# Performance work log

Measured on AMD Instinct MI355X. Metric: run time of the kernel, lower is better.

Reference implementation:

```python
import jax, jax.numpy as jnp
import numpy as np

N, D, H, C = 50000, 256, 4, 16  # nodes, in_dim, heads, out_channels (hidden_dim)
E = 1600000
NEG_SLOPE = 0.2


def _gatv2_layer(x, src, dst, Wl, bl, Wr, br, att, bias, n_nodes):
    """PyG GATv2Conv (share_weights=False, concat=True, eval mode).
    x: [N, Fin]; Wl/Wr: [Fin, H*C]; att: [H, C]; bias: [H*C].
    """
    xl = (x @ Wl + bl).reshape(n_nodes, H, C)  # source-side transform
    xr = (x @ Wr + br).reshape(n_nodes, H, C)  # target-side transform
    # per-edge attention logits: a^T LeakyReLU(xl_j + xr_i)
    e = jax.nn.leaky_relu(xl[src] + xr[dst], negative_slope=NEG_SLOPE)  # [E,H,C]
    logits = jnp.einsum('ehc,hc->eh', e, att)  # [E,H]
    # scatter-softmax over incoming edges of each target node
    m = jax.ops.segment_max(logits, dst, num_segments=n_nodes)  # [N,H]
    ex = jnp.exp(logits - m[dst])
    denom = jax.ops.segment_sum(ex, dst, num_segments=n_nodes)  # [N,H]
    alpha = ex / denom[dst]  # [E,H]
    out = jax.ops.segment_sum(alpha[:, :, None] * xl[src], dst, num_segments=n_nodes)
    return out.reshape(n_nodes, H * C) + bias


def setup_inputs() -> dict:
    key = jax.random.key(0)
    ks = jax.random.split(key, 16)
    g = lambda k, shp, fan: jax.random.normal(k, shp, jnp.float32) * (1.0 / np.sqrt(fan))
    inp = {
        'x': jax.random.normal(ks[0], (N, D), jnp.float32),
        'edge_index': jax.random.randint(ks[1], (2, E), 0, N, dtype=jnp.int64),
        # conv1: in D -> H*C
        'Wl1': g(ks[2], (D, H * C), D), 'bl1': jnp.zeros((H * C,), jnp.float32),
        'Wr1': g(ks[3], (D, H * C), D), 'br1': jnp.zeros((H * C,), jnp.float32),
        'att1': g(ks[4], (H, C), C), 'bias1': jnp.zeros((H * C,), jnp.float32),
        # conv2: in H*C -> H*C
        'Wl2': g(ks[5], (H * C, H * C), H * C), 'bl2': jnp.zeros((H * C,), jnp.float32),
        'Wr2': g(ks[6], (H * C, H * C), H * C), 'br2': jnp.zeros((H * C,), jnp.float32),
        'att2': g(ks[7], (H, C), C), 'bias2': jnp.zeros((H * C,), jnp.float32),
        # output head: H*C -> D
        'Wo': g(ks[8], (H * C, D), H * C), 'bo': jnp.zeros((D,), jnp.float32),
    }
    return inp


def reference(x, edge_index, Wl1, bl1, Wr1, br1, att1, bias1,
              Wl2, bl2, Wr2, br2, att2, bias2, Wo, bo):
    src, dst = edge_index[0], edge_index[1]
    h = jax.nn.relu(_gatv2_layer(x, src, dst, Wl1, bl1, Wr1, br1, att1, bias1, N))
    h = jax.nn.relu(_gatv2_layer(h, src, dst, Wl2, bl2, Wr2, br2, att2, bias2, N))
    return jax.nn.sigmoid(h @ Wo + bo)  # min_max is None -> no affine rescale
```

## Files before the change

### kernel.cpp

```cpp
#include <hip/hip_runtime.h>
#include <math.h>

#define NN 50000
#define DIN 256
#define HC 64
#define NEG 0.2f
#define TM 64
#define NB 196
#define EPB 4096
#define CAP 36864

typedef short bf16x8 __attribute__((ext_vector_type(8)));
typedef unsigned short ush8 __attribute__((ext_vector_type(8)));
typedef float f32x4 __attribute__((ext_vector_type(4)));

__device__ __forceinline__ unsigned short f2bf(float x) {
    unsigned u = __float_as_uint(x);
    u += 0x7FFFu + ((u >> 16) & 1u);
    return (unsigned short)(u >> 16);
}
__device__ __forceinline__ float bf2f(unsigned short h) {
    return __uint_as_float((unsigned)h << 16);
}

template <int CTRL>
__device__ __forceinline__ float dpp_mov(float x) {
    int r = __builtin_amdgcn_update_dpp(0, __float_as_int(x), CTRL, 0xF, 0xF, true);
    return __int_as_float(r);
}


__global__ __launch_bounds__(256) void bhist_k(const int* __restrict__ dst,
                                               int* __restrict__ bcnt, int E) {
    __shared__ int h[NB];
    int t = threadIdx.x;
    for (int i = t; i < NB; i += 256) h[i] = 0;
    __syncthreads();
    int base = blockIdx.x * 2048 + t;
#pragma unroll
    for (int k = 0; k < 8; ++k) {
        int e = base + k * 256;
        if (e < E) atomicAdd(&h[dst[e] >> 8], 1);
    }
    __syncthreads();
    for (int i = t; i < NB; i += 256)
        if (h[i]) atomicAdd(&bcnt[i], h[i]);
}

__global__ __launch_bounds__(256) void bscan_k(const int* __restrict__ bcnt,
                                               int* __restrict__ boffs,
                                               int* __restrict__ bcursor,
                                               int* __restrict__ offs, int E) {
    __shared__ int s[256];
    int t = threadIdx.x;
    s[t] = (t < NB) ? bcnt[t] : 0;
    __syncthreads();
    for (int off = 1; off < 256; off <<= 1) {
        int v = s[t];
        int u = (t >= off) ? s[t - off] : 0;
        __syncthreads();
        s[t] = v + u;
        __syncthreads();
    }
    if (t < NB) {
        int ex = (t == 0) ? 0 : s[t - 1];
        boffs[t] = ex;
        bcursor[t] = ex;
    }
    if (t == NB) boffs[NB] = s[NB - 1];
    if (t == 0) offs[NN] = E;
}

__global__ __launch_bounds__(1024) void bin_k(const int* __restrict__ src,
                                              const int* __restrict__ dst,
                                              int* __restrict__ bcursor,
                                              unsigned* __restrict__ epair, int E) {
    __shared__ int hist[NB];
    __shared__ int lofs[NB];
    __shared__ int gshift[NB];
    __shared__ int scanb[256];
    __shared__ unsigned pbuf[EPB];
    __shared__ unsigned char abkt[EPB];
    int t = threadIdx.x;
    for (int i = t; i < NB; i += 1024) hist[i] = 0;
    __syncthreads();
    int e0 = blockIdx.x * EPB;
    unsigned p[4]; int bk[4], rk[4]; bool val[4];
#pragma unroll
    for (int k = 0; k < 4; ++k) {
        int e = e0 + k * 1024 + t;
        val[k] = e < E;
        if (val[k]) {
            int s = src[e], d = dst[e];
            p[k] = ((unsigned)s << 8) | (unsigned)(d & 255);
            bk[k] = d >> 8;
            rk[k] = atomicAdd(&hist[bk[k]], 1);
        }
    }
    __syncthreads();
    if (t < 256) scanb[t] = (t < NB) ? hist[t] : 0;
    __syncthreads();
    for (int off = 1; off < 256; off <<= 1) {
        int v = 0, u = 0;
        if (t < 256) { v = scanb[t]; if (t >= off) u = scanb[t - off]; }
        __syncthreads();
        if (t < 256) scanb[t] = v + u;
        __syncthreads();
    }
    if (t < NB) {
        int ex = (t == 0) ? 0 : scanb[t - 1];
        lofs[t] = ex;
        int gb = atomicAdd(&bcursor[t], hist[t]);
        gshift[t] = gb - ex;
    }
    __syncthreads();
    int total = scanb[NB - 1];
#pragma unroll
    for (int k = 0; k < 4; ++k) {
        if (val[k]) {
            int pos = lofs[bk[k]] + rk[k];
            pbuf[pos] = p[k];
            abkt[pos] = (unsigned char)bk[k];
        }
    }
    __syncthreads();
    for (int i = t; i < total; i += 1024) {
        int b = abkt[i];
        epair[gshift[b] + i] = pbuf[i];
    }
}

__global__ __launch_bounds__(1024) void bsort_k(const unsigned* __restrict__ epair,
                                                const int* __restrict__ boffs,
                                                int* __restrict__ offs,
                                                unsigned* __restrict__ ssrc, int n) {
    __shared__ int lhist[256];
    __shared__ int lcur[256];
    __shared__ int scanb[256];
    __shared__ unsigned sbuf[CAP];
    int b = blockIdx.x, t = threadIdx.x;
    int start = boffs[b], end = boffs[b + 1];
    int cnt = end - start;
    if (t < 256) lhist[t] = 0;
    __syncthreads();
    for (int i = t; i < cnt; i += 1024) {
        unsigned p = epair[start + i];
        atomicAdd(&lhist[p & 255], 1);
    }
    __syncthreads();
    if (t < 256) scanb[t] = lhist[t];
    __syncthreads();
    for (int off = 1; off < 256; off <<= 1) {
        int v = 0, u = 0;
        if (t < 256) { v = scanb[t]; if (t >= off) u = scanb[t - off]; }
        __syncthreads();
        if (t < 256) scanb[t] = v + u;
        __syncthreads();
    }
    if (t < 256) {
        int ex = (t == 0) ? 0 : scanb[t - 1];
        lcur[t] = ex;
        int node = b * 256 + t;
        if (node < n) offs[node] = start + ex;
    }
    __syncthreads();
    if (cnt <= CAP) {
        for (int i = t; i < cnt; i += 1024) {
            unsigned p = epair[start + i];
            int r = atomicAdd(&lcur[p & 255], 1);
            sbuf[r] = p & ~255u;
        }
        __syncthreads();
        for (int i = t; i < cnt; i += 1024) ssrc[start + i] = sbuf[i];
    } else {
        for (int i = t; i < cnt; i += 1024) {
            unsigned p = epair[start + i];
            int r = atomicAdd(&lcur[p & 255], 1);
            ssrc[start + r] = p & ~255u;
        }
    }
}

__global__ __launch_bounds__(256) void wprep_dual_k(const float* __restrict__ Wl,
                                                    const float* __restrict__ Wr,
                                                    unsigned short* __restrict__ img,
                                                    int K) {
    int i = blockIdx.x * 256 + threadIdx.x;
    int total = (K >> 5) * 10240;
    if (i >= total) return;
    int kk = i % 40;
    int c  = (i / 40) & 127;
    int p  = (i / 5120) & 1;
    int s  = i / 10240;
    unsigned short v = 0;
    if (kk < 32) {
        int k = s * 32 + kk;
        float w = (c < 64) ? Wl[k * HC + c] : Wr[k * HC + (c - 64)];
        unsigned short hi = f2bf(w);
        v = p ? f2bf(w - bf2f(hi)) : hi;
    }
    img[i] = v;
}

__global__ __launch_bounds__(256) void wprep_head_k(const float* __restrict__ Wo,
                                                    unsigned short* __restrict__ img) {
    int i = blockIdx.x * 256 + threadIdx.x;
    if (i >= 40960) return;
    int kk = i % 40;
    int c  = (i / 40) & 127;
    int p  = (i / 5120) & 1;
    int s  = (i / 10240) & 1;
    int h  = i / 20480;
    unsigned short v = 0;
    if (kk < 32) {
        int k = s * 32 + kk;
        float w = Wo[k * DIN + h * 128 + c];
        unsigned short hi = f2bf(w);
        v = p ? f2bf(w - bf2f(hi)) : hi;
    }
    img[i] = v;
}

__global__ __launch_bounds__(256) void gemm_dual_mfma_k(
        const float* __restrict__ A,
        const unsigned short* __restrict__ img,
        const float* __restrict__ bl, const float* __restrict__ br,
        float* __restrict__ xl, float* __restrict__ xr,
        int n, int K) {
    __shared__ __attribute__((aligned(16))) unsigned short As[2][64][40];
    __shared__ __attribute__((aligned(16))) unsigned short Bs[2][128][40];
    int t = threadIdx.x;
    int l = t & 63, w = t >> 6;
    int wr = w >> 1, wc = w & 1;
    int lan = l & 15;
    int kb  = (l >> 4) * 8;
    int row0 = blockIdx.x * 64;
    int srow = t >> 2;
    int skq  = (t & 3) * 8;
    bool rok = (row0 + srow) < n;
    const float* aptr = A + (size_t)(row0 + srow) * K + skq;

    f32x4 acc0[4] = {}, acc1[4] = {};

    int nks = K >> 5;
    for (int ks = 0; ks < nks; ++ks) {
        __syncthreads();
        {
            const ush8* src = (const ush8*)(img + (size_t)ks * 10240);
            ush8* dst = (ush8*)&Bs[0][0][0];
            int base = w * 5 * 64 + l;
#pragma unroll
            for (int c2 = 0; c2 < 5; ++c2) {
                int u = base + c2 * 64;
                dst[u] = src[u];
            }
        }
        {
            float4 f0 = make_float4(0.f, 0.f, 0.f, 0.f), f1 = f0;
            if (rok) {
                f0 = *(const float4*)(aptr + ks * 32);
                f1 = *(const float4*)(aptr + ks * 32 + 4);
            }
            float xs[8] = {f0.x, f0.y, f0.z, f0.w, f1.x, f1.y, f1.z, f1.w};
            ush8 hi8, lo8;
#pragma unroll
            for (int j = 0; j < 8; ++j) {
                unsigned short h = f2bf(xs[j]);
                hi8[j] = h;
                lo8[j] = f2bf(xs[j] - bf2f(h));
            }
            *(ush8*)&As[0][srow][skq] = hi8;
            *(ush8*)&As[1][srow][skq] = lo8;
        }
        __syncthreads();
        bf16x8 ah0 = *(const bf16x8*)&As[0][wr * 32 + lan][kb];
        bf16x8 ah1 = *(const bf16x8*)&As[0][wr * 32 + 16 + lan][kb];
        bf16x8 al0 = *(const bf16x8*)&As[1][wr * 32 + lan][kb];
        bf16x8 al1 = *(const bf16x8*)&As[1][wr * 32 + 16 + lan][kb];
#pragma unroll
        for (int cf = 0; cf < 4; ++cf) {
            int bc = wc * 64 + cf * 16 + lan;
            bf16x8 bhv = *(const bf16x8*)&Bs[0][bc][kb];
            bf16x8 blv = *(const bf16x8*)&Bs[1][bc][kb];
            acc0[cf] = __builtin_amdgcn_mfma_f32_16x16x32_bf16(ah0, bhv, acc0[cf], 0, 0, 0);
            acc1[cf] = __builtin_amdgcn_mfma_f32_16x16x32_bf16(ah1, bhv, acc1[cf], 0, 0, 0);
            acc0[cf] = __builtin_amdgcn_mfma_f32_16x16x32_bf16(al0, bhv, acc0[cf], 0, 0, 0);
            acc1[cf] = __builtin_amdgcn_mfma_f32_16x16x32_bf16(al1, bhv, acc1[cf], 0, 0, 0);
            acc0[cf] = __builtin_amdgcn_mfma_f32_16x16x32_bf16(ah0, blv, acc0[cf], 0, 0, 0);
            acc1[cf] = __builtin_amdgcn_mfma_f32_16x16x32_bf16(ah1, blv, acc1[cf], 0, 0, 0);
        }
    }
#pragma unroll
    for (int cf = 0; cf < 4; ++cf) {
        int col = wc * 64 + cf * 16 + lan;
        float bv; float* dst; int c2;
        if (col < 64) { bv = bl[col]; dst = xl; c2 = col; }
        else          { bv = br[col - 64]; dst = xr; c2 = col - 64; }
#pragma unroll
        for (int rf = 0; rf < 2; ++rf) {
            f32x4 a = rf ? acc1[cf] : acc0[cf];
            int rbase = row0 + wr * 32 + rf * 16 + (l >> 4) * 4;
#pragma unroll
            for (int r = 0; r < 4; ++r) {
                int grow = rbase + r;
                if (grow < n) dst[(size_t)grow * HC + c2] = a[r] + bv;
            }
        }
    }
}

__global__ __launch_bounds__(256) void head_gemm_mfma_k(
        const float* __restrict__ A,
        const unsigned short* __restrict__ img,
        const float* __restrict__ bo,
        float* __restrict__ out, int n) {
    __shared__ __attribute__((aligned(16))) unsigned short As[2][64][40];
    __shared__ __attribute__((aligned(16))) unsigned short Bs[2][128][40];
    int t = threadIdx.x;
    int l = t & 63, w = t >> 6;
    int wr = w >> 1, wc = w & 1;
    int lan = l & 15;
    int kb  = (l >> 4) * 8;
    int row0 = blockIdx.x * 64;
    int coloff = blockIdx.y * 128;
    const unsigned short* himg = img + (size_t)blockIdx.y * 2 * 10240;
    int srow = t >> 2;
    int skq  = (t & 3) * 8;
    bool rok = (row0 + srow) < n;
    const float* aptr = A + (size_t)(row0 + srow) * HC + skq;

    f32x4 acc0[4] = {}, acc1[4] = {};

    for (int ks = 0; ks < 2; ++ks) {
        __syncthreads();
        {
            const ush8* src = (const ush8*)(himg + (size_t)ks * 10240);
            ush8* dst = (ush8*)&Bs[0][0][0];
            int base = w * 5 * 64 + l;
#pragma unroll
            for (int c2 = 0; c2 < 5; ++c2) {
                int u = base + c2 * 64;
                dst[u] = src[u];
            }
        }
        {
            float4 f0 = make_float4(0.f, 0.f, 0.f, 0.f), f1 = f0;
            if (rok) {
                f0 = *(const float4*)(aptr + ks * 32);
                f1 = *(const float4*)(aptr + ks * 32 + 4);
            }
            float xs[8] = {f0.x, f0.y, f0.z, f0.w, f1.x, f1.y, f1.z, f1.w};
            ush8 hi8, lo8;
#pragma unroll
            for (int j = 0; j < 8; ++j) {
                unsigned short h = f2bf(xs[j]);
                hi8[j] = h;
                lo8[j] = f2bf(xs[j] - bf2f(h));
            }
            *(ush8*)&As[0][srow][skq] = hi8;
            *(ush8*)&As[1][srow][skq] = lo8;
        }
        __syncthreads();
        bf16x8 ah0 = *(const bf16x8*)&As[0][wr * 32 + lan][kb];
        bf16x8 ah1 = *(const bf16x8*)&As[0][wr * 32 + 16 + lan][kb];
        bf16x8 al0 = *(const bf16x8*)&As[1][wr * 32 + lan][kb];
        bf16x8 al1 = *(const bf16x8*)&As[1][wr * 32 + 16 + lan][kb];
#pragma unroll
        for (int cf = 0; cf < 4; ++cf) {
            int bc = wc * 64 + cf * 16 + lan;
            bf16x8 bhv = *(const bf16x8*)&Bs[0][bc][kb];
            bf16x8 blv = *(const bf16x8*)&Bs[1][bc][kb];
            acc0[cf] = __builtin_amdgcn_mfma_f32_16x16x32_bf16(ah0, bhv, acc0[cf], 0, 0, 0);
            acc1[cf] = __builtin_amdgcn_mfma_f32_16x16x32_bf16(ah1, bhv, acc1[cf], 0, 0, 0);
            acc0[cf] = __builtin_amdgcn_mfma_f32_16x16x32_bf16(al0, bhv, acc0[cf], 0, 0, 0);
            acc1[cf] = __builtin_amdgcn_mfma_f32_16x16x32_bf16(al1, bhv, acc1[cf], 0, 0, 0);
            acc0[cf] = __builtin_amdgcn_mfma_f32_16x16x32_bf16(ah0, blv, acc0[cf], 0, 0, 0);
            acc1[cf] = __builtin_amdgcn_mfma_f32_16x16x32_bf16(ah1, blv, acc1[cf], 0, 0, 0);
        }
    }
#pragma unroll
    for (int cf = 0; cf < 4; ++cf) {
        int col = coloff + wc * 64 + cf * 16 + lan;
        float bv = bo[col];
#pragma unroll
        for (int rf = 0; rf < 2; ++rf) {
            f32x4 a = rf ? acc1[cf] : acc0[cf];
            int rbase = row0 + wr * 32 + rf * 16 + (l >> 4) * 4;
#pragma unroll
            for (int r = 0; r < 4; ++r) {
                int grow = rbase + r;
                if (grow < n) {
                    float v = a[r] + bv;
                    out[(size_t)grow * DIN + col] = 1.f / (1.f + __expf(-v));
                }
            }
        }
    }
}

#define AGRP(EBASE, FULL)                                                     \
    {                                                                         \
        int e = (EBASE) + q;                                                  \
        bool ok = FULL ? true : (e < hi);                                     \
        int ec = FULL ? e : (ok ? e : (hi - 1));                              \
        unsigned sb = ssb[ec];                                                \
        float4 xv = *(const float4*)(xlb + sb + loff);                        \
        float s0 = xv.x + xrq.x, s1 = xv.y + xrq.y;                           \
        float s2 = xv.z + xrq.z, s3 = xv.w + xrq.w;                           \
        float tt = atq.x * fmaxf(s0, NEG * s0);                               \
        tt = fmaf(atq.y, fmaxf(s1, NEG * s1), tt);                            \
        tt = fmaf(atq.z, fmaxf(s2, NEG * s2), tt);                            \
        tt = fmaf(atq.w, fmaxf(s3, NEG * s3), tt);                            \
        tt += dpp_mov<0xB1>(tt);                                              \
        tt += dpp_mov<0x4E>(tt);                                              \
        float ex = exp2f(tt);                                                 \
        if (!FULL) ex = ok ? ex : 0.f;                                        \
        den += ex;                                                            \
        acc.x = fmaf(ex, xv.x, acc.x); acc.y = fmaf(ex, xv.y, acc.y);         \
        acc.z = fmaf(ex, xv.z, acc.z); acc.w = fmaf(ex, xv.w, acc.w);         \
    }

__global__ __launch_bounds__(256) void agg_k(const float* __restrict__ xl,
                                             const float* __restrict__ xr,
                                             const float* __restrict__ att,
                                             const float* __restrict__ bias,
                                             const int* __restrict__ offs,
                                             const unsigned* __restrict__ ssb,
                                             float* __restrict__ out, int n) {
    int wave = (blockIdx.x * 256 + threadIdx.x) >> 6;
    int lane = threadIdx.x & 63;
    if (wave >= n) return;
    int q  = lane >> 4;
    int sl = lane & 15;
    const char* xlb = (const char*)xl;
    unsigned loff = (unsigned)sl * 16u;
    float4 xrq = *(const float4*)(xr + (size_t)wave * HC + sl * 4);
    float4 atq = *(const float4*)(att + sl * 4);
    const float LOG2E = 1.44269504088896340736f;
    atq.x *= LOG2E; atq.y *= LOG2E; atq.z *= LOG2E; atq.w *= LOG2E;
    float4 acc = make_float4(0.f, 0.f, 0.f, 0.f);
    float den = 0.f;
    int lo = __builtin_amdgcn_readfirstlane(offs[wave]);
    int hi = __builtin_amdgcn_readfirstlane(offs[wave + 1]);
    int i = lo;
    for (; i + 16 <= hi; i += 16) {
        AGRP(i, true) AGRP(i + 4, true) AGRP(i + 8, true) AGRP(i + 12, true)
    }
    for (; i < hi; i += 4) {
        AGRP(i, false)
    }
#pragma unroll
    for (int m = 16; m < 64; m <<= 1) {
        acc.x += __shfl_xor(acc.x, m);
        acc.y += __shfl_xor(acc.y, m);
        acc.z += __shfl_xor(acc.z, m);
        acc.w += __shfl_xor(acc.w, m);
        den   += __shfl_xor(den, m);
    }
    if (q == 0) {
        float r = (den > 0.f) ? 1.f / den : 0.f;
        float4 b4 = *(const float4*)(bias + sl * 4);
        float4 o;
        o.x = fmaxf(fmaf(acc.x, r, b4.x), 0.f);
        o.y = fmaxf(fmaf(acc.y, r, b4.y), 0.f);
        o.z = fmaxf(fmaf(acc.z, r, b4.z), 0.f);
        o.w = fmaxf(fmaf(acc.w, r, b4.w), 0.f);
        *(float4*)(out + (size_t)wave * HC + sl * 4) = o;
    }
}

extern "C" void kernel_launch(void* const* d_in, const int* in_sizes, int n_in,
                              void* d_out, int out_size, void* d_ws, size_t ws_size,
                              hipStream_t stream) {
    const float* x    = (const float*)d_in[0];
    const int*   ei   = (const int*)d_in[1];
    const float* Wl1  = (const float*)d_in[2];
    const float* bl1  = (const float*)d_in[3];
    const float* Wr1  = (const float*)d_in[4];
    const float* br1  = (const float*)d_in[5];
    const float* att1 = (const float*)d_in[6];
    const float* bias1= (const float*)d_in[7];
    const float* Wl2  = (const float*)d_in[8];
    const float* bl2  = (const float*)d_in[9];
    const float* Wr2  = (const float*)d_in[10];
    const float* br2  = (const float*)d_in[11];
    const float* att2 = (const float*)d_in[12];
    const float* bias2= (const float*)d_in[13];
    const float* Wo   = (const float*)d_in[14];
    const float* bo   = (const float*)d_in[15];
    float* out = (float*)d_out;

    int E = in_sizes[1] / 2;
    const int* srcv = ei;
    const int* dstv = ei + E;

    size_t NF = (size_t)NN * HC;
    float* xl = (float*)d_ws;
    float* xr = xl + NF;
    float* hb = xr + NF;
    int* offs        = (int*)(hb + NF);
    unsigned* ssrc   = (unsigned*)(offs + NN + 1);
    int* boffs   = (int*)(ssrc + E);
    int* bcursor = boffs + NB + 1;
    int* bcnt    = bcursor + NB;
    unsigned* epair = (unsigned*)d_out;
    unsigned short* img1 = (unsigned short*)d_out;
    unsigned short* img2 = img1 + 81920;
    unsigned short* imgh = (unsigned short*)xl;

    hipMemsetAsync(bcnt, 0, NB * sizeof(int), stream);
    bhist_k<<<(E + 2047) / 2048, 256, 0, stream>>>(dstv, bcnt, E);
    bscan_k<<<1, 256, 0, stream>>>(bcnt, boffs, bcursor, offs, E);
    bin_k<<<(E + EPB - 1) / EPB, 1024, 0, stream>>>(srcv, dstv, bcursor, epair, E);
    bsort_k<<<NB, 1024, 0, stream>>>(epair, boffs, offs, ssrc, NN);
    wprep_dual_k<<<320, 256, 0, stream>>>(Wl1, Wr1, img1, DIN);
    wprep_dual_k<<<80, 256, 0, stream>>>(Wl2, Wr2, img2, HC);

    int gb = (NN + TM - 1) / TM;
    gemm_dual_mfma_k<<<gb, 256, 0, stream>>>(x, img1, bl1, br1, xl, xr, NN, DIN);
    agg_k<<<(NN + 3) / 4, 256, 0, stream>>>(xl, xr, att1, bias1, offs, ssrc, hb, NN);
    gemm_dual_mfma_k<<<gb, 256, 0, stream>>>(hb, img2, bl2, br2, xl, xr, NN, HC);
    agg_k<<<(NN + 3) / 4, 256, 0, stream>>>(xl, xr, att2, bias2, offs, ssrc, hb, NN);
    wprep_head_k<<<160, 256, 0, stream>>>(Wo, imgh);
    head_gemm_mfma_k<<<dim3(gb, 2), 256, 0, stream>>>(hb, imgh, bo, out, NN);
}
```

Measured before the change: 350.6 us.

## Store source-side features as fp16 and batch edge index loads with shuffles

The GEMM now writes the source-side transform xl as fp16 into a scratch region of the output buffer, and the sorted source offsets are halved to match the smaller row stride. The aggregation kernel gathers 8-byte fp16 chunks instead of 16-byte fp32 ones and loads up to 32 edge indices per wave at once, handing them out with shuffles. This roughly halves the random gather traffic, which dominates the edge aggregation. The cost is reduced precision for xl in both the attention logits and the weighted sum, and reliance on the output buffer being free at that offset.

```diff
diff --git a/kernel.cpp b/kernel.cpp
--- a/kernel.cpp
+++ b/kernel.cpp
@@ -171,12 +171,12 @@
             sbuf[r] = p & ~255u;
         }
         __syncthreads();
-        for (int i = t; i < cnt; i += 1024) ssrc[start + i] = sbuf[i];
+        for (int i = t; i < cnt; i += 1024) ssrc[start + i] = sbuf[i] >> 1;
     } else {
         for (int i = t; i < cnt; i += 1024) {
             unsigned p = epair[start + i];
             int r = atomicAdd(&lcur[p & 255], 1);
-            ssrc[start + r] = p & ~255u;
+            ssrc[start + r] = (p & ~255u) >> 1;
         }
     }
 }
@@ -225,7 +225,7 @@
         const float* __restrict__ A,
         const unsigned short* __restrict__ img,
         const float* __restrict__ bl, const float* __restrict__ br,
-        float* __restrict__ xl, float* __restrict__ xr,
+        _Float16* __restrict__ xlh, float* __restrict__ xr,
         int n, int K) {
     __shared__ __attribute__((aligned(16))) unsigned short As[2][64][40];
     __shared__ __attribute__((aligned(16))) unsigned short Bs[2][128][40];
@@ -293,9 +293,9 @@
 #pragma unroll
     for (int cf = 0; cf < 4; ++cf) {
         int col = wc * 64 + cf * 16 + lan;
-        float bv; float* dst; int c2;
-        if (col < 64) { bv = bl[col]; dst = xl; c2 = col; }
-        else          { bv = br[col - 64]; dst = xr; c2 = col - 64; }
+        bool left = col < 64;
+        float bv = left ? bl[col] : br[col - 64];
+        int c2 = left ? col : col - 64;
 #pragma unroll
         for (int rf = 0; rf < 2; ++rf) {
             f32x4 a = rf ? acc1[cf] : acc0[cf];
@@ -303,7 +303,11 @@
 #pragma unroll
             for (int r = 0; r < 4; ++r) {
                 int grow = rbase + r;
-                if (grow < n) dst[(size_t)grow * HC + c2] = a[r] + bv;
+                if (grow < n) {
+                    float v = a[r] + bv;
+                    if (left) xlh[(size_t)grow * HC + c2] = (_Float16)v;
+                    else      xr[(size_t)grow * HC + c2] = v;
+                }
             }
         }
     }
@@ -398,15 +402,16 @@
     }
 }
 
-#define AGRP(EBASE, FULL)                                                     \
+union H4 { uint2 u; _Float16 h[4]; };
+
+#define AGRP_BODY(SB)                                                         \
     {                                                                         \
-        int e = (EBASE) + q;                                                  \
-        bool ok = FULL ? true : (e < hi);                                     \
-        int ec = FULL ? e : (ok ? e : (hi - 1));                              \
-        unsigned sb = ssb[ec];                                                \
-        float4 xv = *(const float4*)(xlb + sb + loff);                        \
-        float s0 = xv.x + xrq.x, s1 = xv.y + xrq.y;                           \
-        float s2 = xv.z + xrq.z, s3 = xv.w + xrq.w;                           \
+        H4 cv;                                                                \
+        cv.u = *(const uint2*)(xhb + (SB) + hoff);                            \
+        float xv0 = (float)cv.h[0], xv1 = (float)cv.h[1];                     \
+        float xv2 = (float)cv.h[2], xv3 = (float)cv.h[3];                     \
+        float s0 = xv0 + xrq.x, s1 = xv1 + xrq.y;                             \
+        float s2 = xv2 + xrq.z, s3 = xv3 + xrq.w;                             \
         float tt = atq.x * fmaxf(s0, NEG * s0);                               \
         tt = fmaf(atq.y, fmaxf(s1, NEG * s1), tt);                            \
         tt = fmaf(atq.z, fmaxf(s2, NEG * s2), tt);                            \
@@ -414,13 +419,18 @@
         tt += dpp_mov<0xB1>(tt);                                              \
         tt += dpp_mov<0x4E>(tt);                                              \
         float ex = exp2f(tt);                                                 \
-        if (!FULL) ex = ok ? ex : 0.f;                                        \
         den += ex;                                                            \
-        acc.x = fmaf(ex, xv.x, acc.x); acc.y = fmaf(ex, xv.y, acc.y);         \
-        acc.z = fmaf(ex, xv.z, acc.z); acc.w = fmaf(ex, xv.w, acc.w);         \
-    }
-
-__global__ __launch_bounds__(256) void agg_k(const float* __restrict__ xl,
+        acc.x = fmaf(ex, xv0, acc.x); acc.y = fmaf(ex, xv1, acc.y);           \
+        acc.z = fmaf(ex, xv2, acc.z); acc.w = fmaf(ex, xv3, acc.w);           \
+    }
+
+#define AGRPS(KK)                                                             \
+    {                                                                         \
+        unsigned sb = (unsigned)__shfl((int)sbv, (KK) * 4 + q);               \
+        AGRP_BODY(sb)                                                         \
+    }
+
+__global__ __launch_bounds__(256) void agg_k(const _Float16* __restrict__ xlh,
                                              const float* __restrict__ xr,
                                              const float* __restrict__ att,
                                              const float* __restrict__ bias,
@@ -432,8 +442,8 @@
     if (wave >= n) return;
     int q  = lane >> 4;
     int sl = lane & 15;
-    const char* xlb = (const char*)xl;
-    unsigned loff = (unsigned)sl * 16u;
+    const char* xhb = (const char*)xlh;
+    unsigned hoff = (unsigned)sl * 8u;
     float4 xrq = *(const float4*)(xr + (size_t)wave * HC + sl * 4);
     float4 atq = *(const float4*)(att + sl * 4);
     const float LOG2E = 1.44269504088896340736f;
@@ -443,11 +453,37 @@
     int lo = __builtin_amdgcn_readfirstlane(offs[wave]);
     int hi = __builtin_amdgcn_readfirstlane(offs[wave + 1]);
     int i = lo;
+    for (; i + 32 <= hi; i += 32) {
+        unsigned sbv = ssb[i + (lane & 31)];
+        AGRPS(0) AGRPS(1) AGRPS(2) AGRPS(3)
+        AGRPS(4) AGRPS(5) AGRPS(6) AGRPS(7)
+    }
     for (; i + 16 <= hi; i += 16) {
-        AGRP(i, true) AGRP(i + 4, true) AGRP(i + 8, true) AGRP(i + 12, true)
+        unsigned sbv = ssb[i + (lane & 15)];
+        AGRPS(0) AGRPS(1) AGRPS(2) AGRPS(3)
     }
     for (; i < hi; i += 4) {
-        AGRP(i, false)
+        int e = i + q;
+        bool ok = e < hi;
+        int ec = ok ? e : (hi - 1);
+        unsigned sb = ssb[ec];
+        H4 cv;
+        cv.u = *(const uint2*)(xhb + sb + hoff);
+        float xv0 = (float)cv.h[0], xv1 = (float)cv.h[1];
+        float xv2 = (float)cv.h[2], xv3 = (float)cv.h[3];
+        float s0 = xv0 + xrq.x, s1 = xv1 + xrq.y;
+        float s2 = xv2 + xrq.z, s3 = xv3 + xrq.w;
+        float tt = atq.x * fmaxf(s0, NEG * s0);
+        tt = fmaf(atq.y, fmaxf(s1, NEG * s1), tt);
+        tt = fmaf(atq.z, fmaxf(s2, NEG * s2), tt);
+        tt = fmaf(atq.w, fmaxf(s3, NEG * s3), tt);
+        tt += dpp_mov<0xB1>(tt);
+        tt += dpp_mov<0x4E>(tt);
+        float ex = exp2f(tt);
+        ex = ok ? ex : 0.f;
+        den += ex;
+        acc.x = fmaf(ex, xv0, acc.x); acc.y = fmaf(ex, xv1, acc.y);
+        acc.z = fmaf(ex, xv2, acc.z); acc.w = fmaf(ex, xv3, acc.w);
     }
 #pragma unroll
     for (int m = 16; m < 64; m <<= 1) {
@@ -507,6 +543,7 @@
     unsigned short* img1 = (unsigned short*)d_out;
     unsigned short* img2 = img1 + 81920;
     unsigned short* imgh = (unsigned short*)xl;
+    _Float16* xlh = (_Float16*)((char*)d_out + (16u << 20));
 
     hipMemsetAsync(bcnt, 0, NB * sizeof(int), stream);
     bhist_k<<<(E + 2047) / 2048, 256, 0, stream>>>(dstv, bcnt, E);
@@ -517,10 +554,10 @@
     wprep_dual_k<<<80, 256, 0, stream>>>(Wl2, Wr2, img2, HC);
 
     int gb = (NN + TM - 1) / TM;
-    gemm_dual_mfma_k<<<gb, 256, 0, stream>>>(x, img1, bl1, br1, xl, xr, NN, DIN);
-    agg_k<<<(NN + 3) / 4, 256, 0, stream>>>(xl, xr, att1, bias1, offs, ssrc, hb, NN);
-    gemm_dual_mfma_k<<<gb, 256, 0, stream>>>(hb, img2, bl2, br2, xl, xr, NN, HC);
-    agg_k<<<(NN + 3) / 4, 256, 0, stream>>>(xl, xr, att2, bias2, offs, ssrc, hb, NN);
+    gemm_dual_mfma_k<<<gb, 256, 0, stream>>>(x, img1, bl1, br1, xlh, xr, NN, DIN);
+    agg_k<<<(NN + 3) / 4, 256, 0, stream>>>(xlh, xr, att1, bias1, offs, ssrc, hb, NN);
+    gemm_dual_mfma_k<<<gb, 256, 0, stream>>>(hb, img2, bl2, br2, xlh, xr, NN, HC);
+    agg_k<<<(NN + 3) / 4, 256, 0, stream>>>(xlh, xr, att2, bias2, offs, ssrc, hb, NN);
     wprep_head_k<<<160, 256, 0, stream>>>(Wo, imgh);
     head_gemm_mfma_k<<<dim3(gb, 2), 256, 0, stream>>>(hb, imgh, bo, out, NN);
 }
```

Measured after the change: 319.7 us. 8.8% less time.
